# Optimization experiments

Hardware: AMD Instinct MI355X
Metric: run time of the kernel (lower is better)

Reference implementation:

```python
import jax, jax.numpy as jnp
import numpy as np

IN_CHANNELS = 128
NUM_OUTPUTS = 4
BATCH_SIZE = 4096
N_NODES = 500000


def setup_inputs() -> dict:
    key = jax.random.key(0)
    ks = jax.random.split(key, 8)
    C = IN_CHANNELS
    k = jax.random.normal(ks[0], (N_NODES, C), dtype=jnp.float32)
    v = jax.random.normal(ks[1], (N_NODES, C), dtype=jnp.float32)
    h = jax.random.normal(ks[2], (BATCH_SIZE * C,), dtype=jnp.float32)
    batch = jnp.sort(jax.random.randint(ks[3], (N_NODES,), 0, BATCH_SIZE)).astype(jnp.int64)
    s = 1.0 / np.sqrt(C)
    # torch LSTM params: input size 2C, hidden C, gate order (i, f, g, o)
    W_ih = jax.random.uniform(ks[4], (4 * C, 2 * C), minval=-s, maxval=s, dtype=jnp.float32)
    W_hh = jax.random.uniform(ks[5], (4 * C, C), minval=-s, maxval=s, dtype=jnp.float32)
    b_ih = jax.random.uniform(ks[6], (4 * C,), minval=-s, maxval=s, dtype=jnp.float32)
    b_hh = jax.random.uniform(ks[7], (4 * C,), minval=-s, maxval=s, dtype=jnp.float32)
    return {"k": k, "v": v, "h": h, "W_ih": W_ih, "W_hh": W_hh,
            "b_ih": b_ih, "b_hh": b_hh, "batch": batch}


def _lstm_cell(x, h0, c0, W_ih, W_hh, b_ih, b_hh):
    C = h0.shape[-1]
    gates = x @ W_ih.T + b_ih + h0 @ W_hh.T + b_hh  # [B, 4C]
    i, f, g, o = jnp.split(gates, 4, axis=-1)
    c = jax.nn.sigmoid(f) * c0 + jax.nn.sigmoid(i) * jnp.tanh(g)
    h = jax.nn.sigmoid(o) * jnp.tanh(c)
    return h, c


def reference(k, v, h, W_ih, W_hh, b_ih, b_hh, batch):
    C = k.shape[-1]
    B = h.shape[0] // C  # num_layers=1
    batch = batch.astype(jnp.int32)
    h0 = h.reshape(B, C)
    c0 = h.reshape(B, C)
    q_star = jnp.zeros((B, 2 * C), dtype=v.dtype)
    readouts = []
    for _ in range(NUM_OUTPUTS):
        h0, c0 = _lstm_cell(q_star, h0, c0, W_ih, W_hh, b_ih, b_hh)
        q = h0  # [B, C]
        e = jnp.sum(k * q[batch], axis=-1)  # [N]
        m = jax.ops.segment_max(e, batch, num_segments=B, indices_are_sorted=True)
        ex = jnp.exp(e - m[batch])
        s = jax.ops.segment_sum(ex, batch, num_segments=B, indices_are_sorted=True)
        a = ex / (s[batch] + 1e-16)  # segment softmax
        r = jax.ops.segment_sum(a[:, None] * v, batch, num_segments=B, indices_are_sorted=True)  # [B, C]
        readouts.append(r)
        q_star = jnp.concatenate([q, r], axis=-1)
    return jnp.concatenate(readouts, axis=-1)  # [B, C*NUM_OUTPUTS]
```

## Files before the change

kernel.cpp:

```cpp
#include <hip/hip_runtime.h>
#include <math.h>

#define C 128
#define B 4096
#define NNODES 500000
#define NOUT 4
#define KTOT 384


__global__ void init_state(const float* __restrict__ h, float* __restrict__ h0,
                           float* __restrict__ c0, float* __restrict__ q_star,
                           int* __restrict__ seg_start, int* __restrict__ seg_end) {
    int idx = blockIdx.x * blockDim.x + threadIdx.x;
    if (idx < B * 2 * C) q_star[idx] = 0.f;
    if (idx < B * C) { float t = h[idx]; h0[idx] = t; c0[idx] = t; }
    if (idx < B)     { seg_start[idx] = 0; seg_end[idx] = 0; }
}

__global__ void seg_bounds(const int* __restrict__ batch, int* __restrict__ seg_start,
                           int* __restrict__ seg_end) {
    int n = blockIdx.x * blockDim.x + threadIdx.x;
    if (n >= NNODES) return;
    int b = batch[n];
    if (n == 0 || batch[n - 1] != b) seg_start[b] = n;
    if (n == NNODES - 1 || batch[n + 1] != b) seg_end[b] = n + 1;
}

#define BM 64
#define BN 64
#define BK 16
#define LDP 68

__global__ __launch_bounds__(256) void lstm_gemm(
    const float* __restrict__ q_star, const float* __restrict__ h0,
    const float* __restrict__ W_ih, const float* __restrict__ W_hh,
    const float* __restrict__ b_ih, const float* __restrict__ b_hh,
    float* __restrict__ gates) {
    __shared__ float As[BK][LDP];
    __shared__ float Bs[BK][LDP];

    const int bm0 = blockIdx.x * BM;
    const int jn0 = blockIdx.y * BN;
    const int tid = threadIdx.x;
    const int tx = tid & 15;
    const int ty = tid >> 4;

    const int st_row = tid >> 2;
    const int st_k   = (tid & 3) << 2;

    float acc[4][4] = {{0.f}};

    for (int k0 = 0; k0 < KTOT; k0 += BK) {
        float4 av, bv;
        {
            const int gb = bm0 + st_row;
            if (k0 < 256)
                av = *(const float4*)(q_star + (size_t)gb * 256 + (k0 + st_k));
            else
                av = *(const float4*)(h0 + (size_t)gb * 128 + (k0 - 256 + st_k));
            const int gj = jn0 + st_row;
            if (k0 < 256)
                bv = *(const float4*)(W_ih + (size_t)gj * 256 + (k0 + st_k));
            else
                bv = *(const float4*)(W_hh + (size_t)gj * 128 + (k0 - 256 + st_k));
        }
        __syncthreads();
        As[st_k + 0][st_row] = av.x;
        As[st_k + 1][st_row] = av.y;
        As[st_k + 2][st_row] = av.z;
        As[st_k + 3][st_row] = av.w;
        Bs[st_k + 0][st_row] = bv.x;
        Bs[st_k + 1][st_row] = bv.y;
        Bs[st_k + 2][st_row] = bv.z;
        Bs[st_k + 3][st_row] = bv.w;
        __syncthreads();

#pragma unroll
        for (int kk = 0; kk < BK; ++kk) {
            const float4 a4 = *(const float4*)&As[kk][ty << 2];
            const float4 b4 = *(const float4*)&Bs[kk][tx << 2];
            const float a[4] = {a4.x, a4.y, a4.z, a4.w};
            const float bb[4] = {b4.x, b4.y, b4.z, b4.w};
#pragma unroll
            for (int i = 0; i < 4; ++i)
#pragma unroll
                for (int j = 0; j < 4; ++j)
                    acc[i][j] = fmaf(a[i], bb[j], acc[i][j]);
        }
    }

    const int jj = jn0 + (tx << 2);
    const float4 bi = *(const float4*)(b_ih + jj);
    const float4 bh = *(const float4*)(b_hh + jj);
    const float bias[4] = {bi.x + bh.x, bi.y + bh.y, bi.z + bh.z, bi.w + bh.w};
#pragma unroll
    for (int i = 0; i < 4; ++i) {
        const int gb = bm0 + (ty << 2) + i;
        float4 o;
        o.x = acc[i][0] + bias[0];
        o.y = acc[i][1] + bias[1];
        o.z = acc[i][2] + bias[2];
        o.w = acc[i][3] + bias[3];
        *(float4*)(gates + (size_t)gb * (4 * C) + jj) = o;
    }
}

__global__ void lstm_act(const float* __restrict__ gates, float* __restrict__ c0,
                         float* __restrict__ h0, float* __restrict__ q_star) {
    int idx = blockIdx.x * blockDim.x + threadIdx.x;
    if (idx >= B * C) return;
    int b = idx / C, c = idx % C;
    const float* g = gates + (size_t)b * 4 * C;
    float ii = g[c];
    float ff = g[C + c];
    float gg = g[2 * C + c];
    float oo = g[3 * C + c];
    float si = 1.f / (1.f + __expf(-ii));
    float sf = 1.f / (1.f + __expf(-ff));
    float so = 1.f / (1.f + __expf(-oo));
    float tg = tanhf(gg);
    float cn = sf * c0[idx] + si * tg;
    float hn = so * tanhf(cn);
    c0[idx] = cn;
    h0[idx] = hn;
    q_star[(size_t)b * 2 * C + c] = hn;
}

__global__ __launch_bounds__(256) void attention(
    const float* __restrict__ k, const float* __restrict__ v,
    const float* __restrict__ h0, const int* __restrict__ seg_start,
    const int* __restrict__ seg_end, float* __restrict__ q_star,
    float* __restrict__ out, int t) {
    const int b = blockIdx.x;
    const int tid = threadIdx.x;
    const int wave = tid >> 6;
    const int lane = tid & 63;

    __shared__ float q_s[C];
    __shared__ float m_w[4], s_w[4];
    __shared__ float racc[4][C];

    if (tid < C) q_s[tid] = h0[(size_t)b * C + tid];
    __syncthreads();

    const int s0 = seg_start[b];
    const int s1 = seg_end[b];
    const float qa = q_s[lane * 2];
    const float qb = q_s[lane * 2 + 1];

    float m = -INFINITY, ssum = 0.f, acc0 = 0.f, acc1 = 0.f;

    for (int n = s0 + wave; n < s1; n += 4) {
        const float2 kk = *(const float2*)(k + (size_t)n * C + lane * 2);
        float part = kk.x * qa + kk.y * qb;
#pragma unroll
        for (int off = 32; off >= 1; off >>= 1) part += __shfl_xor(part, off);
        const float2 vv = *(const float2*)(v + (size_t)n * C + lane * 2);
        const float mn = fmaxf(m, part);
        const float sc = __expf(m - mn);
        const float p  = __expf(part - mn);
        ssum = ssum * sc + p;
        acc0 = acc0 * sc + p * vv.x;
        acc1 = acc1 * sc + p * vv.y;
        m = mn;
    }

    if (lane == 0) { m_w[wave] = m; s_w[wave] = ssum; }
    racc[wave][lane * 2]     = acc0;
    racc[wave][lane * 2 + 1] = acc1;
    __syncthreads();

    if (tid < C) {
        const float M = fmaxf(fmaxf(m_w[0], m_w[1]), fmaxf(m_w[2], m_w[3]));
        float S = 0.f, R = 0.f;
#pragma unroll
        for (int w = 0; w < 4; ++w) {
            const float sc = (m_w[w] == -INFINITY) ? 0.f : __expf(m_w[w] - M);
            S = fmaf(s_w[w], sc, S);
            R = fmaf(racc[w][tid], sc, R);
        }
        const float r = R / (S + 1e-16f);
        out[(size_t)b * (NOUT * C) + t * C + tid] = r;
        q_star[(size_t)b * 2 * C + C + tid] = r;
    }
}

extern "C" void kernel_launch(void* const* d_in, const int* in_sizes, int n_in,
                              void* d_out, int out_size, void* d_ws, size_t ws_size,
                              hipStream_t stream) {
    const float* k    = (const float*)d_in[0];
    const float* v    = (const float*)d_in[1];
    const float* h    = (const float*)d_in[2];
    const float* W_ih = (const float*)d_in[3];
    const float* W_hh = (const float*)d_in[4];
    const float* b_ih = (const float*)d_in[5];
    const float* b_hh = (const float*)d_in[6];
    const int*   batch = (const int*)d_in[7];
    float* out = (float*)d_out;

    float* ws      = (float*)d_ws;
    float* h0      = ws;
    float* c0      = h0 + (size_t)B * C;
    float* q_star  = c0 + (size_t)B * C;
    float* gates   = q_star + (size_t)B * 2 * C;
    int*   sstart  = (int*)(gates + (size_t)B * 4 * C);
    int*   send    = sstart + B;

    init_state<<<(B * 2 * C + 255) / 256, 256, 0, stream>>>(h, h0, c0, q_star, sstart, send);
    seg_bounds<<<(NNODES + 255) / 256, 256, 0, stream>>>(batch, sstart, send);

    for (int t = 0; t < NOUT; ++t) {
        lstm_gemm<<<dim3(B / BM, (4 * C) / BN), 256, 0, stream>>>(
            q_star, h0, W_ih, W_hh, b_ih, b_hh, gates);
        lstm_act<<<(B * C + 255) / 256, 256, 0, stream>>>(gates, c0, h0, q_star);
        attention<<<B, 256, 0, stream>>>(k, v, h0, sstart, send, q_star, out, t);
    }
}
```

Measured before the change: 964.7 us.

## Split attention into three-pass segment softmax with wider per-node vector loads

Replaces the single-pass online softmax with three passes: compute scores and the segment max (storing scores to a workspace), then the exp-sum, then the normalized weighted sum over v. Each node is now handled by a 16-lane group using float4 loads, so four nodes are processed per wave, with shorter shuffle reductions and no per-node rescaling exps. This removes the serial rescale dependency and the full-wave reductions, but adds a global score buffer and extra barriers, and the k and v reads are now split across separate passes.

```diff
diff --git a/kernel.cpp b/kernel.cpp
--- a/kernel.cpp
+++ b/kernel.cpp
@@ -129,57 +129,78 @@
 __global__ __launch_bounds__(256) void attention(
     const float* __restrict__ k, const float* __restrict__ v,
     const float* __restrict__ h0, const int* __restrict__ seg_start,
-    const int* __restrict__ seg_end, float* __restrict__ q_star,
-    float* __restrict__ out, int t) {
+    const int* __restrict__ seg_end, float* __restrict__ e_ws,
+    float* __restrict__ q_star, float* __restrict__ out, int t) {
     const int b = blockIdx.x;
     const int tid = threadIdx.x;
-    const int wave = tid >> 6;
+    const int w = tid >> 6;
     const int lane = tid & 63;
-
-    __shared__ float q_s[C];
-    __shared__ float m_w[4], s_w[4];
-    __shared__ float racc[4][C];
-
-    if (tid < C) q_s[tid] = h0[(size_t)b * C + tid];
-    __syncthreads();
+    const int g = lane >> 4;
+    const int j = lane & 15;
+    const int ch = j << 3;
+
+    __shared__ float red[4];
+    __shared__ float racc[16][C];
 
     const int s0 = seg_start[b];
     const int s1 = seg_end[b];
-    const float qa = q_s[lane * 2];
-    const float qb = q_s[lane * 2 + 1];
-
-    float m = -INFINITY, ssum = 0.f, acc0 = 0.f, acc1 = 0.f;
-
-    for (int n = s0 + wave; n < s1; n += 4) {
-        const float2 kk = *(const float2*)(k + (size_t)n * C + lane * 2);
-        float part = kk.x * qa + kk.y * qb;
-#pragma unroll
-        for (int off = 32; off >= 1; off >>= 1) part += __shfl_xor(part, off);
-        const float2 vv = *(const float2*)(v + (size_t)n * C + lane * 2);
-        const float mn = fmaxf(m, part);
-        const float sc = __expf(m - mn);
-        const float p  = __expf(part - mn);
-        ssum = ssum * sc + p;
-        acc0 = acc0 * sc + p * vv.x;
-        acc1 = acc1 * sc + p * vv.y;
-        m = mn;
-    }
-
-    if (lane == 0) { m_w[wave] = m; s_w[wave] = ssum; }
-    racc[wave][lane * 2]     = acc0;
-    racc[wave][lane * 2 + 1] = acc1;
+
+    const float4 qa = *(const float4*)(h0 + (size_t)b * C + ch);
+    const float4 qb = *(const float4*)(h0 + (size_t)b * C + ch + 4);
+
+    float m = -INFINITY;
+    for (int n0 = s0 + w * 4; n0 < s1; n0 += 16) {
+        const int n = n0 + g;
+        if (n < s1) {
+            const float4 ka = *(const float4*)(k + (size_t)n * C + ch);
+            const float4 kb = *(const float4*)(k + (size_t)n * C + ch + 4);
+            float part = ka.x * qa.x + ka.y * qa.y + ka.z * qa.z + ka.w * qa.w
+                       + kb.x * qb.x + kb.y * qb.y + kb.z * qb.z + kb.w * qb.w;
+            part += __shfl_xor(part, 1);
+            part += __shfl_xor(part, 2);
+            part += __shfl_xor(part, 4);
+            part += __shfl_xor(part, 8);
+            if (j == 0) e_ws[n] = part;
+            m = fmaxf(m, part);
+        }
+    }
+    m = fmaxf(m, __shfl_xor(m, 16));
+    m = fmaxf(m, __shfl_xor(m, 32));
+    if (lane == 0) red[w] = m;
+    __syncthreads();
+    const float M = fmaxf(fmaxf(red[0], red[1]), fmaxf(red[2], red[3]));
+    __syncthreads();
+
+    float s = 0.f;
+    for (int n = s0 + tid; n < s1; n += 256) s += __expf(e_ws[n] - M);
+#pragma unroll
+    for (int off = 32; off >= 1; off >>= 1) s += __shfl_xor(s, off);
+    if (lane == 0) red[w] = s;
+    __syncthreads();
+    const float S = red[0] + red[1] + red[2] + red[3];
+    const float inv = 1.f / (S + 1e-16f);
+
+    float4 A0 = {0.f, 0.f, 0.f, 0.f}, A1 = {0.f, 0.f, 0.f, 0.f};
+    for (int n0 = s0 + w * 4; n0 < s1; n0 += 16) {
+        const int n = n0 + g;
+        if (n < s1) {
+            const float p = __expf(e_ws[n] - M) * inv;
+            const float4 va = *(const float4*)(v + (size_t)n * C + ch);
+            const float4 vb = *(const float4*)(v + (size_t)n * C + ch + 4);
+            A0.x = fmaf(p, va.x, A0.x); A0.y = fmaf(p, va.y, A0.y);
+            A0.z = fmaf(p, va.z, A0.z); A0.w = fmaf(p, va.w, A0.w);
+            A1.x = fmaf(p, vb.x, A1.x); A1.y = fmaf(p, vb.y, A1.y);
+            A1.z = fmaf(p, vb.z, A1.z); A1.w = fmaf(p, vb.w, A1.w);
+        }
+    }
+    *(float4*)&racc[(w << 2) + g][ch]     = A0;
+    *(float4*)&racc[(w << 2) + g][ch + 4] = A1;
     __syncthreads();
 
     if (tid < C) {
-        const float M = fmaxf(fmaxf(m_w[0], m_w[1]), fmaxf(m_w[2], m_w[3]));
-        float S = 0.f, R = 0.f;
-#pragma unroll
-        for (int w = 0; w < 4; ++w) {
-            const float sc = (m_w[w] == -INFINITY) ? 0.f : __expf(m_w[w] - M);
-            S = fmaf(s_w[w], sc, S);
-            R = fmaf(racc[w][tid], sc, R);
-        }
-        const float r = R / (S + 1e-16f);
+        float r = 0.f;
+#pragma unroll
+        for (int p = 0; p < 16; ++p) r += racc[p][tid];
         out[(size_t)b * (NOUT * C) + t * C + tid] = r;
         q_star[(size_t)b * 2 * C + C + tid] = r;
     }
@@ -203,7 +224,8 @@
     float* c0      = h0 + (size_t)B * C;
     float* q_star  = c0 + (size_t)B * C;
     float* gates   = q_star + (size_t)B * 2 * C;
-    int*   sstart  = (int*)(gates + (size_t)B * 4 * C);
+    float* e_ws    = gates + (size_t)B * 4 * C;
+    int*   sstart  = (int*)(e_ws + NNODES);
     int*   send    = sstart + B;
 
     init_state<<<(B * 2 * C + 255) / 256, 256, 0, stream>>>(h, h0, c0, q_star, sstart, send);
@@ -213,6 +235,6 @@
         lstm_gemm<<<dim3(B / BM, (4 * C) / BN), 256, 0, stream>>>(
             q_star, h0, W_ih, W_hh, b_ih, b_hh, gates);
         lstm_act<<<(B * C + 255) / 256, 256, 0, stream>>>(gates, c0, h0, q_star);
-        attention<<<B, 256, 0, stream>>>(k, v, h0, sstart, send, q_star, out, t);
-    }
-}
+        attention<<<B, 256, 0, stream>>>(k, v, h0, sstart, send, e_ws, q_star, out, t);
+    }
+}
```

Measured after the change: 957.8 us. Within noise of the previous version (-0.7%).
